# Performance work log

Measured on AMD Instinct MI355X. Metric: run time of the kernel, lower is better.

Reference implementation:

```python
import math
import jax, jax.numpy as jnp
import numpy as np

IN_DIM, OUT_DIM = 256, 128
IN_SEQ, OUT_SEQ = 512, 512
NUM_BASIS = 16
LN_EPS = 1e-5
TWO_PI = 2.0 * math.pi


def _make_periods():
    # periods[i, j, g] = i*(out_dim*num_basis) + j*num_basis + g + 2
    i = np.arange(OUT_DIM)[:, None, None]
    j = np.arange(OUT_DIM)[None, :, None]
    g = np.arange(NUM_BASIS)[None, None, :]
    return jnp.asarray((i * (OUT_DIM * NUM_BASIS) + j * NUM_BASIS + g + 2).astype(np.float32))


def setup_inputs() -> dict:
    key = jax.random.key(0)
    kx, kM, kP, kL = jax.random.split(key, 4)
    x = jax.random.normal(kx, (IN_SEQ, IN_DIM), dtype=jnp.float32)
    M = jax.random.normal(kM, (OUT_DIM, IN_DIM), dtype=jnp.float32) * 0.5
    P = jax.random.normal(kP, (OUT_DIM, OUT_DIM, NUM_BASIS), dtype=jnp.float32) * 0.1
    Linker = jax.random.normal(kL, (IN_SEQ, OUT_SEQ), dtype=jnp.float32) * 0.1
    gamma = jnp.ones((OUT_DIM,), dtype=jnp.float32)
    beta = jnp.zeros((OUT_DIM,), dtype=jnp.float32)
    periods = _make_periods()  # (O, O, B) constant buffer
    return {"x": x, "M": M, "P": P, "Linker": Linker,
            "gamma": gamma, "beta": beta, "periods": periods}


def reference(x, M, P, Linker, gamma, beta, periods):
    # Projection: Z = x @ M.T  -> (S, O)
    Z = x @ M.T
    # LayerNorm over last dim
    mu = jnp.mean(Z, axis=-1, keepdims=True)
    var = jnp.mean(jnp.square(Z - mu), axis=-1, keepdims=True)
    Zn = (Z - mu) * jax.lax.rsqrt(var + LN_EPS) * gamma + beta
    # Position transform: T[k,i] = sum_{j,g} Zn[k,j] * P[i,j,g] * cos(2*pi*k / periods[i,j,g])
    k = jnp.arange(Z.shape[0], dtype=jnp.float32)[:, None, None, None]  # (S,1,1,1)
    phi = jnp.cos(TWO_PI * k / periods)  # (S, O, O, B)
    T = jnp.einsum('kj,ijg,kijg->ki', Zn, P, phi)  # (S, O)
    # Sequence transform: U = Linker.T @ T -> (out_seq, O)
    U = Linker.T @ T
    # 'shared' residual uses pre-LayerNorm projection x @ M.T
    residual = Linker.T @ Z
    return U + residual
```

## Files before the change

### kernel.cpp

```cpp
#include <hip/hip_runtime.h>

#define IN_DIM   256
#define OUT_DIM  128
#define IN_SEQ   512
#define OUT_SEQ  512
#define NUM_BASIS 16
#define LN_EPS   1e-5f

__global__ __launch_bounds__(256) void kA(const float* __restrict__ x,
                                          const float* __restrict__ M,
                                          const float* __restrict__ gamma,
                                          const float* __restrict__ beta,
                                          float* __restrict__ Zn,
                                          float* __restrict__ ZT) {
  const int k = blockIdx.x;
  const int t = threadIdx.x;
  __shared__ __align__(16) float xk[IN_DIM];
  __shared__ float red[256];
  __shared__ float stats[8];

  xk[t] = x[k * IN_DIM + t];
  __syncthreads();

  const int j = t & 127;
  const int h = t >> 7;
  const float4* __restrict__ M4 = reinterpret_cast<const float4*>(M + j * IN_DIM + h * 128);
  const float4* __restrict__ x4 = reinterpret_cast<const float4*>(xk + h * 128);
  float acc = 0.f;
#pragma unroll 8
  for (int c = 0; c < 32; ++c) {
    float4 m = M4[c];
    float4 xv = x4[c];
    acc = fmaf(m.x, xv.x, acc);
    acc = fmaf(m.y, xv.y, acc);
    acc = fmaf(m.z, xv.z, acc);
    acc = fmaf(m.w, xv.w, acc);
  }
  red[t] = acc;
  __syncthreads();

  float z = 0.f;
  if (t < 128) z = red[t] + red[t + 128];

  float s1 = (t < 128) ? z : 0.f;
  float s2 = (t < 128) ? z * z : 0.f;
#pragma unroll
  for (int m = 1; m < 64; m <<= 1) {
    s1 += __shfl_xor(s1, m);
    s2 += __shfl_xor(s2, m);
  }
  const int w = t >> 6;
  if ((t & 63) == 0) {
    stats[w] = s1;
    stats[4 + w] = s2;
  }
  __syncthreads();
  const float mu  = (stats[0] + stats[1] + stats[2] + stats[3]) * (1.f / 128.f);
  const float msq = (stats[4] + stats[5] + stats[6] + stats[7]) * (1.f / 128.f);
  const float rs  = rsqrtf(msq - mu * mu + LN_EPS);

  if (t < 128) {
    float zn = (z - mu) * rs * gamma[t] + beta[t];
    Zn[k * OUT_DIM + t] = zn;
    ZT[t * IN_SEQ + k] = z;
  }
}

__global__ __launch_bounds__(256) void kB(const float* __restrict__ P,
                                          const float* __restrict__ Zn,
                                          const float* __restrict__ ZT,
                                          float* __restrict__ V) {
  const int i  = blockIdx.y;
  const int k0 = blockIdx.x * 64;
  const int t  = threadIdx.x;

  __shared__ float2 pairs[OUT_DIM * NUM_BASIS];
  __shared__ float zn_lds[64 * 129];
  __shared__ float red[64 * 5];

  const float* __restrict__ Pi = P + i * (OUT_DIM * NUM_BASIS);
  const int pbase = i * (OUT_DIM * NUM_BASIS) + 2;
#pragma unroll
  for (int e = t; e < OUT_DIM * NUM_BASIS; e += 256) {
    float pw = Pi[e];
    float pinv = 1.0f / (float)(pbase + e);
    pairs[e] = make_float2(pw, pinv);
  }
#pragma unroll
  for (int m = 0; m < 32; ++m) {
    int idx = m * 256 + t;
    int r = idx >> 7;
    int j = idx & 127;
    zn_lds[r * 129 + j] = Zn[(k0 + r) * OUT_DIM + j];
  }
  __syncthreads();

  const int kl = t & 63;
  const int jq = t >> 6;
  const float kf = (float)(k0 + kl);
  const float* __restrict__ znrow = zn_lds + kl * 129;

  float acc = 0.f;
  for (int j = jq * 32; j < jq * 32 + 32; ++j) {
    float z = znrow[j];
    const float2* __restrict__ pp = pairs + j * NUM_BASIS;
    float accj = 0.f;
#pragma unroll
    for (int g = 0; g < NUM_BASIS; ++g) {
      float2 wv = pp[g];
      float ang = kf * wv.y;
      float fr  = __builtin_amdgcn_fractf(ang);
      float c   = __builtin_amdgcn_cosf(fr);
      accj = fmaf(wv.x, c, accj);
    }
    acc = fmaf(z, accj, acc);
  }

  red[kl * 5 + jq] = acc;
  __syncthreads();
  if (t < 64) {
    float s = red[t * 5 + 0] + red[t * 5 + 1] + red[t * 5 + 2] + red[t * 5 + 3];
    const int k = k0 + t;
    V[k * OUT_DIM + i] = s + ZT[i * IN_SEQ + k];
  }
}

__global__ __launch_bounds__(256) void kC(const float* __restrict__ L,
                                          const float* __restrict__ V,
                                          float* __restrict__ out) {
  const int t = threadIdx.x;
  const int s = blockIdx.x * 2 + (t >> 7);
  const int i = t & 127;
  const int k0 = blockIdx.y * 128;
  float acc = 0.f;
#pragma unroll 8
  for (int kk = 0; kk < 128; ++kk) {
    const int k = k0 + kk;
    acc = fmaf(L[k * OUT_SEQ + s], V[k * OUT_DIM + i], acc);
  }
  atomicAdd(&out[s * OUT_DIM + i], acc);
}

extern "C" void kernel_launch(void* const* d_in, const int* in_sizes, int n_in,
                              void* d_out, int out_size, void* d_ws, size_t ws_size,
                              hipStream_t stream) {
  const float* x      = (const float*)d_in[0];
  const float* M      = (const float*)d_in[1];
  const float* P      = (const float*)d_in[2];
  const float* Linker = (const float*)d_in[3];
  const float* gamma  = (const float*)d_in[4];
  const float* beta   = (const float*)d_in[5];
  float* out = (float*)d_out;

  float* ws = (float*)d_ws;
  float* Zn = ws;
  float* ZT = ws + IN_SEQ * OUT_DIM;
  float* V  = ws + 2 * IN_SEQ * OUT_DIM;

  hipMemsetAsync(d_out, 0, (size_t)out_size * sizeof(float), stream);

  kA<<<dim3(IN_SEQ), dim3(256), 0, stream>>>(x, M, gamma, beta, Zn, ZT);
  kB<<<dim3(8, OUT_DIM), dim3(256), 0, stream>>>(P, Zn, ZT, V);
  kC<<<dim3(OUT_SEQ / 2, 4), dim3(256), 0, stream>>>(Linker, V, out);
}
```

Measured before the change: 52.04 us.

## Split position transform over basis pairs with atomics, drop output memset

The position-transform kernel now parallelises over pairs of basis functions: each block handles one output column and two basis indices for all 512 positions, reading Zn transposed and atomically accumulating into V, which already holds the residual Z. This removes the LDS staging of P pairs and Zn rows and the in-block reduction. The sequence GEMM now reduces its two halves of k in shared memory and writes the output directly, so the memset and output atomics are gone. The trade-off is many atomics into V and recomputing reciprocals per element.

```diff
diff --git a/kernel.cpp b/kernel.cpp
--- a/kernel.cpp
+++ b/kernel.cpp
@@ -7,12 +7,16 @@
 #define NUM_BASIS 16
 #define LN_EPS   1e-5f
 
-__global__ __launch_bounds__(256) void kA(const float* __restrict__ x,
-                                          const float* __restrict__ M,
-                                          const float* __restrict__ gamma,
-                                          const float* __restrict__ beta,
-                                          float* __restrict__ Zn,
-                                          float* __restrict__ ZT) {
+__device__ __forceinline__ float cosrev(float x) {
+  return __builtin_amdgcn_cosf(__builtin_amdgcn_fractf(x));
+}
+
+__global__ __launch_bounds__(256) void k_prep(const float* __restrict__ x,
+                                              const float* __restrict__ M,
+                                              const float* __restrict__ gamma,
+                                              const float* __restrict__ beta,
+                                              float* __restrict__ ZnT,
+                                              float* __restrict__ V) {
   const int k = blockIdx.x;
   const int t = threadIdx.x;
   __shared__ __align__(16) float xk[IN_DIM];
@@ -24,7 +28,8 @@
 
   const int j = t & 127;
   const int h = t >> 7;
-  const float4* __restrict__ M4 = reinterpret_cast<const float4*>(M + j * IN_DIM + h * 128);
+  const float4* __restrict__ M4 =
+      reinterpret_cast<const float4*>(M + j * IN_DIM + h * 128);
   const float4* __restrict__ x4 = reinterpret_cast<const float4*>(xk + h * 128);
   float acc = 0.f;
 #pragma unroll 8
@@ -61,84 +66,67 @@
 
   if (t < 128) {
     float zn = (z - mu) * rs * gamma[t] + beta[t];
-    Zn[k * OUT_DIM + t] = zn;
-    ZT[t * IN_SEQ + k] = z;
+    ZnT[t * IN_SEQ + k] = zn;
+    V[k * OUT_DIM + t]  = z;
   }
 }
 
-__global__ __launch_bounds__(256) void kB(const float* __restrict__ P,
-                                          const float* __restrict__ Zn,
-                                          const float* __restrict__ ZT,
-                                          float* __restrict__ V) {
+__global__ __launch_bounds__(256) void k_pos(const float* __restrict__ P,
+                                             const float* __restrict__ ZnT,
+                                             float* __restrict__ V) {
+  const int gp = blockIdx.x;
   const int i  = blockIdx.y;
-  const int k0 = blockIdx.x * 64;
   const int t  = threadIdx.x;
+  const float kf0 = (float)t;
+  const float kf1 = (float)(t + 256);
+  const int g0 = gp * 2;
+  const int pbase = i * (OUT_DIM * NUM_BASIS) + g0 + 2;
+  const float* __restrict__ Prow = P + (size_t)i * OUT_DIM * NUM_BASIS + g0;
 
-  __shared__ float2 pairs[OUT_DIM * NUM_BASIS];
-  __shared__ float zn_lds[64 * 129];
-  __shared__ float red[64 * 5];
+  float acc0 = 0.f, acc1 = 0.f;
+#pragma unroll 2
+  for (int j = 0; j < OUT_DIM; ++j) {
+    const float z0 = ZnT[j * IN_SEQ + t];
+    const float z1 = ZnT[j * IN_SEQ + t + 256];
+    {
+      const float pinv = __builtin_amdgcn_rcpf((float)(pbase + j * 16));
+      const float Pw = Prow[j * NUM_BASIS];
+      acc0 = fmaf(Pw * z0, cosrev(kf0 * pinv), acc0);
+      acc1 = fmaf(Pw * z1, cosrev(kf1 * pinv), acc1);
+    }
+    {
+      const float pinv = __builtin_amdgcn_rcpf((float)(pbase + j * 16 + 1));
+      const float Pw = Prow[j * NUM_BASIS + 1];
+      acc0 = fmaf(Pw * z0, cosrev(kf0 * pinv), acc0);
+      acc1 = fmaf(Pw * z1, cosrev(kf1 * pinv), acc1);
+    }
+  }
+  atomicAdd(&V[(size_t)t * OUT_DIM + i], acc0);
+  atomicAdd(&V[(size_t)(t + 256) * OUT_DIM + i], acc1);
+}
 
-  const float* __restrict__ Pi = P + i * (OUT_DIM * NUM_BASIS);
-  const int pbase = i * (OUT_DIM * NUM_BASIS) + 2;
-#pragma unroll
-  for (int e = t; e < OUT_DIM * NUM_BASIS; e += 256) {
-    float pw = Pi[e];
-    float pinv = 1.0f / (float)(pbase + e);
-    pairs[e] = make_float2(pw, pinv);
+__global__ __launch_bounds__(256) void k_seq(const float* __restrict__ L,
+                                             const float* __restrict__ V,
+                                             float* __restrict__ out) {
+  const int s = blockIdx.x;
+  const int t = threadIdx.x;
+  const int i = t & 127;
+  const int q = t >> 7;
+  __shared__ float red[2 * OUT_DIM];
+
+  const int k0 = q * 256;
+  float acc = 0.f;
+#pragma unroll 8
+  for (int kk = 0; kk < 256; ++kk) {
+    const int k = k0 + kk;
+    acc = fmaf(L[(size_t)k * OUT_SEQ + s],
+               V[(size_t)k * OUT_DIM + i], acc);
   }
-#pragma unroll
-  for (int m = 0; m < 32; ++m) {
-    int idx = m * 256 + t;
-    int r = idx >> 7;
-    int j = idx & 127;
-    zn_lds[r * 129 + j] = Zn[(k0 + r) * OUT_DIM + j];
-  }
+  red[q * OUT_DIM + i] = acc;
   __syncthreads();
 
-  const int kl = t & 63;
-  const int jq = t >> 6;
-  const float kf = (float)(k0 + kl);
-  const float* __restrict__ znrow = zn_lds + kl * 129;
-
-  float acc = 0.f;
-  for (int j = jq * 32; j < jq * 32 + 32; ++j) {
-    float z = znrow[j];
-    const float2* __restrict__ pp = pairs + j * NUM_BASIS;
-    float accj = 0.f;
-#pragma unroll
-    for (int g = 0; g < NUM_BASIS; ++g) {
-      float2 wv = pp[g];
-      float ang = kf * wv.y;
-      float fr  = __builtin_amdgcn_fractf(ang);
-      float c   = __builtin_amdgcn_cosf(fr);
-      accj = fmaf(wv.x, c, accj);
-    }
-    acc = fmaf(z, accj, acc);
-  }
-
-  red[kl * 5 + jq] = acc;
-  __syncthreads();
-  if (t < 64) {
-    float s = red[t * 5 + 0] + red[t * 5 + 1] + red[t * 5 + 2] + red[t * 5 + 3];
-    const int k = k0 + t;
-    V[k * OUT_DIM + i] = s + ZT[i * IN_SEQ + k];
-  }
-}
-
-__global__ __launch_bounds__(256) void kC(const float* __restrict__ L,
-                                          const float* __restrict__ V,
-                                          float* __restrict__ out) {
-  const int t = threadIdx.x;
-  const int s = blockIdx.x * 2 + (t >> 7);
-  const int i = t & 127;
-  const int k0 = blockIdx.y * 128;
-  float acc = 0.f;
-#pragma unroll 8
-  for (int kk = 0; kk < 128; ++kk) {
-    const int k = k0 + kk;
-    acc = fmaf(L[k * OUT_SEQ + s], V[k * OUT_DIM + i], acc);
-  }
-  atomicAdd(&out[s * OUT_DIM + i], acc);
+  if (t < OUT_DIM)
+    out[(size_t)s * OUT_DIM + t] = red[t] + red[OUT_DIM + t];
 }
 
 extern "C" void kernel_launch(void* const* d_in, const int* in_sizes, int n_in,
@@ -152,14 +140,11 @@
   const float* beta   = (const float*)d_in[5];
   float* out = (float*)d_out;
 
-  float* ws = (float*)d_ws;
-  float* Zn = ws;
-  float* ZT = ws + IN_SEQ * OUT_DIM;
-  float* V  = ws + 2 * IN_SEQ * OUT_DIM;
+  float* ws  = (float*)d_ws;
+  float* ZnT = ws;
+  float* V   = ws + OUT_DIM * IN_SEQ;
 
-  hipMemsetAsync(d_out, 0, (size_t)out_size * sizeof(float), stream);
-
-  kA<<<dim3(IN_SEQ), dim3(256), 0, stream>>>(x, M, gamma, beta, Zn, ZT);
-  kB<<<dim3(8, OUT_DIM), dim3(256), 0, stream>>>(P, Zn, ZT, V);
-  kC<<<dim3(OUT_SEQ / 2, 4), dim3(256), 0, stream>>>(Linker, V, out);
+  k_prep<<<dim3(IN_SEQ), dim3(256), 0, stream>>>(x, M, gamma, beta, ZnT, V);
+  k_pos<<<dim3(NUM_BASIS / 2, OUT_DIM), dim3(256), 0, stream>>>(P, ZnT, V);
+  k_seq<<<dim3(OUT_SEQ), dim3(256), 0, stream>>>(Linker, V, out);
 }
```

After: 72.25 us. 1.39x slower.
